# Performance work log

Measured on AMD Instinct MI355X. Metric: run time of the kernel, lower is better.

Reference implementation:

```python
import jax, jax.numpy as jnp
import numpy as np

N = 50000      # nodes
E = 800000     # random edges (self-loops appended -> E + N total)
IN, HID, OUT, HEADS = 128, 256, 256, 8


def _gat_layer(x, src, dst, W, a_src, a_dst, bias):
    # x: [N, F_in]; W: [F_in, H*C]; a_src/a_dst: [H, C]; bias: [H*C]
    n = x.shape[0]
    H, C = a_src.shape
    h = (x @ W).reshape(n, H, C)                      # per-head transform
    al_s = jnp.sum(h * a_src, axis=-1)                # [N, H]
    al_d = jnp.sum(h * a_dst, axis=-1)                # [N, H]
    e = jax.nn.leaky_relu(al_s[src] + al_d[dst], 0.2) # [E, H]
    # segmented softmax over incoming edges of each destination node
    m = jax.ops.segment_max(e, dst, num_segments=n)   # [N, H]
    e = jnp.exp(e - m[dst])
    s = jax.ops.segment_sum(e, dst, num_segments=n)   # [N, H]
    alpha = e / (s[dst] + 1e-16)                      # [E, H]
    out = jax.ops.segment_sum(alpha[:, :, None] * h[src], dst, num_segments=n)
    return out.reshape(n, H * C) + bias


def setup_inputs() -> dict:
    key = jax.random.key(0)
    ks = jax.random.split(key, 9)
    x = jax.random.normal(ks[0], (N, IN), dtype=jnp.float32)
    src = jax.random.randint(ks[1], (E,), 0, N)
    dst = jax.random.randint(ks[2], (E,), 0, N)
    loop = jnp.arange(N)  # PyG GATConv adds self-loops by default
    edge_index = jnp.stack([jnp.concatenate([src, loop]),
                            jnp.concatenate([dst, loop])]).astype(jnp.int64)
    C1, C2 = HID // HEADS, OUT // HEADS
    W1 = jax.random.normal(ks[3], (IN, HID), jnp.float32) * (1.0 / np.sqrt(IN))
    a1_src = jax.random.normal(ks[4], (HEADS, C1), jnp.float32) * 0.1
    a1_dst = jax.random.normal(ks[5], (HEADS, C1), jnp.float32) * 0.1
    b1 = jnp.zeros((HID,), jnp.float32)
    W2 = jax.random.normal(ks[6], (HID, OUT), jnp.float32) * (1.0 / np.sqrt(HID))
    a2_src = jax.random.normal(ks[7], (HEADS, C2), jnp.float32) * 0.1
    a2_dst = jax.random.normal(ks[8], (HEADS, C2), jnp.float32) * 0.1
    b2 = jnp.zeros((OUT,), jnp.float32)
    return {"x": x, "edge_index": edge_index,
            "W1": W1, "a1_src": a1_src, "a1_dst": a1_dst, "b1": b1,
            "W2": W2, "a2_src": a2_src, "a2_dst": a2_dst, "b2": b2}


def reference(x, edge_index, W1, a1_src, a1_dst, b1, W2, a2_src, a2_dst, b2):
    src, dst = edge_index[0], edge_index[1]
    h = jax.nn.elu(_gat_layer(x, src, dst, W1, a1_src, a1_dst, b1))
    out = jax.nn.elu(_gat_layer(h, src, dst, W2, a2_src, a2_dst, b2))
    return out
```

## Files before the change

### kernel.cpp

```cpp
#include <hip/hip_runtime.h>
#include <hip/hip_bf16.h>


#define HEADS 8
#define F 256

typedef _Float16 h8 __attribute__((ext_vector_type(8)));
typedef _Float16 h4 __attribute__((ext_vector_type(4)));
typedef float f4 __attribute__((ext_vector_type(4)));


__global__ void k_prep(const float* __restrict__ W1, _Float16* __restrict__ Wt1,
                       const float* __restrict__ W2, _Float16* __restrict__ Wt2,
                       const int* __restrict__ dst, int Et, int* __restrict__ deg) {
  int b = blockIdx.x, tid = threadIdx.x;
  if (b < 128) {
    Wt1[(size_t)tid * 128 + b] = (_Float16)W1[(size_t)b * F + tid];
  } else if (b < 384) {
    int k = b - 128;
    Wt2[(size_t)tid * 256 + k] = (_Float16)W2[(size_t)k * F + tid];
  } else {
    int i = (b - 384) * 256 + tid;
    for (; i < Et; i += 512 * 256) atomicAdd(&deg[dst[i]], 1);
  }
}


__global__ __launch_bounds__(1024) void k_scan1(const int* __restrict__ deg, int n,
                                                int* __restrict__ rowptr, int* __restrict__ bsum) {
  __shared__ int s[1024];
  int i = blockIdx.x * 1024 + threadIdx.x;
  int v = (i < n) ? ((deg[i] + 3) & ~3) : 0;
  s[threadIdx.x] = v;
  __syncthreads();
  for (int off = 1; off < 1024; off <<= 1) {
    int add = (threadIdx.x >= off) ? s[threadIdx.x - off] : 0;
    __syncthreads();
    s[threadIdx.x] += add;
    __syncthreads();
  }
  if (i < n) rowptr[i] = s[threadIdx.x] - v;
  if (threadIdx.x == 1023) bsum[blockIdx.x] = s[1023];
}

__global__ void k_scan23(int n, const int* __restrict__ bsum,
                         int* __restrict__ rowptr, int* __restrict__ rowwork) {
  __shared__ int boffs;
  int nbx = blockIdx.x >> 2;
  if (threadIdx.x < 64) {
    int t = threadIdx.x;
    int v = (t < nbx) ? bsum[t] : 0;
#pragma unroll
    for (int off = 32; off; off >>= 1) v += __shfl_xor(v, off, 64);
    if (t == 0) boffs = v;
  }
  __syncthreads();
  int i = blockIdx.x * 256 + threadIdx.x;
  if (i < n) {
    int v = rowptr[i] + boffs;
    rowptr[i] = v;
    rowwork[i] = v;
  }
}


template <bool AF32, bool FILL>
__global__ __launch_bounds__(512) void k_gemm(const void* __restrict__ Av,
                                              const _Float16* __restrict__ Bt,
                                              _Float16* __restrict__ C,
                                              const float* __restrict__ a_src,
                                              const float* __restrict__ a_dst,
                                              float* __restrict__ als,
                                              float* __restrict__ ald,
                                              int M, int K,
                                              const int* __restrict__ esrc,
                                              const int* __restrict__ edst,
                                              int Et, int* __restrict__ rowwork,
                                              int* __restrict__ csr, int gemmBlocks) {
  if (FILL && (int)blockIdx.x >= gemmBlocks) {
    int i = ((int)blockIdx.x - gemmBlocks) * 512 + threadIdx.x;
    int stride = ((int)gridDim.x - gemmBlocks) * 512;
    for (; i < Et; i += stride) {
      int pos = atomicAdd(&rowwork[edst[i]], 1);
      csr[pos] = esrc[i];
    }
    return;
  }

  __shared__ _Float16 As[128][40];
  __shared__ _Float16 Bs[256][40];
  int tid = threadIdx.x;
  int lane = tid & 63, w = tid >> 6;
  int wr = w & 1, wc = w >> 1;
  int rowBase = blockIdx.x * 128;
  f4 acc[4][4] = {};

  int arow = tid >> 2, akoff = (tid & 3) * 8;
  int arow_g = min(rowBase + arow, M - 1);
  const _Float16* Ap = (const _Float16*)Av + (size_t)arow_g * K + akoff;
  const float*    Apf = (const float*)Av + (size_t)arow_g * K + akoff;
  int bc = tid >> 1, bkoff = (tid & 1) * 16;
  const _Float16* Bp = Bt + (size_t)bc * K + bkoff;

  int kl = (lane >> 4) * 8;
  int rl = lane & 15;

  int nsteps = K >> 5;
  h8 av;
  float4 af0, af1;
  if (AF32) { af0 = *(const float4*)(Apf); af1 = *(const float4*)(Apf + 4); }
  else av = *(const h8*)(Ap);
  h8 bv0 = *(const h8*)(Bp);
  h8 bv1 = *(const h8*)(Bp + 8);

  for (int s = 0; s < nsteps; ++s) {
    if (AF32) {
      h8 t = {(_Float16)af0.x, (_Float16)af0.y, (_Float16)af0.z, (_Float16)af0.w,
              (_Float16)af1.x, (_Float16)af1.y, (_Float16)af1.z, (_Float16)af1.w};
      *(h8*)&As[arow][akoff] = t;
    } else {
      *(h8*)&As[arow][akoff] = av;
    }
    *(h8*)&Bs[bc][bkoff] = bv0;
    *(h8*)&Bs[bc][bkoff + 8] = bv1;
    __syncthreads();
    if (s + 1 < nsteps) {
      int k0 = (s + 1) << 5;
      if (AF32) { af0 = *(const float4*)(Apf + k0); af1 = *(const float4*)(Apf + k0 + 4); }
      else av = *(const h8*)(Ap + k0);
      bv0 = *(const h8*)(Bp + k0);
      bv1 = *(const h8*)(Bp + k0 + 8);
    }
    h8 afr[4], bfr[4];
#pragma unroll
    for (int fi = 0; fi < 4; ++fi) afr[fi] = *(const h8*)&As[wr * 64 + fi * 16 + rl][kl];
#pragma unroll
    for (int fj = 0; fj < 4; ++fj) bfr[fj] = *(const h8*)&Bs[wc * 64 + fj * 16 + rl][kl];
#pragma unroll
    for (int fi = 0; fi < 4; ++fi)
#pragma unroll
      for (int fj = 0; fj < 4; ++fj)
        acc[fi][fj] = __builtin_amdgcn_mfma_f32_16x16x32_f16(afr[fi], bfr[fj], acc[fi][fj], 0, 0, 0);
    __syncthreads();
  }

  int rquad = (lane >> 4) * 4;

#pragma unroll
  for (int fi = 0; fi < 4; ++fi)
#pragma unroll
    for (int fj = 0; fj < 4; ++fj) {
      int col = wc * 64 + fj * 16 + rl;
#pragma unroll
      for (int r = 0; r < 4; ++r) {
        int row = rowBase + wr * 64 + fi * 16 + rquad + r;
        if (row < M) C[(size_t)row * F + col] = (_Float16)acc[fi][fj][r];
      }
    }

  int head0 = wc * 2;
  float as0 = a_src[head0 * 32 + rl],      as1 = a_src[head0 * 32 + 16 + rl];
  float ad0 = a_dst[head0 * 32 + rl],      ad1 = a_dst[head0 * 32 + 16 + rl];
  float cs0 = a_src[head0 * 32 + 32 + rl], cs1 = a_src[head0 * 32 + 48 + rl];
  float cd0 = a_dst[head0 * 32 + 32 + rl], cd1 = a_dst[head0 * 32 + 48 + rl];
#pragma unroll
  for (int fi = 0; fi < 4; ++fi)
#pragma unroll
    for (int r = 0; r < 4; ++r) {
      float v0s = acc[fi][0][r] * as0 + acc[fi][1][r] * as1;
      float v0d = acc[fi][0][r] * ad0 + acc[fi][1][r] * ad1;
      float v1s = acc[fi][2][r] * cs0 + acc[fi][3][r] * cs1;
      float v1d = acc[fi][2][r] * cd0 + acc[fi][3][r] * cd1;
#pragma unroll
      for (int off = 8; off; off >>= 1) {
        v0s += __shfl_xor(v0s, off);
        v0d += __shfl_xor(v0d, off);
        v1s += __shfl_xor(v1s, off);
        v1d += __shfl_xor(v1d, off);
      }
      int row = rowBase + wr * 64 + fi * 16 + rquad + r;
      if (rl == 0 && row < M) {
        als[row * HEADS + head0] = v0s;
        ald[row * HEADS + head0] = v0d;
        als[row * HEADS + head0 + 1] = v1s;
        ald[row * HEADS + head0 + 1] = v1d;
      }
    }
}


template <bool F16OUT>
__global__ __launch_bounds__(256) void k_agg(const int* __restrict__ rowptr,
                                             const int* __restrict__ deg,
                                             const int* __restrict__ csr,
                                             const float* __restrict__ al_s,
                                             const float* __restrict__ al_d,
                                             const _Float16* __restrict__ h,
                                             const float* __restrict__ bias,
                                             float* __restrict__ outf,
                                             _Float16* __restrict__ outh,
                                             int n) {
  int tid = threadIdx.x;
  int w = tid >> 6, lane = tid & 63;
  int node = blockIdx.x * 4 + w;
  if (node >= n) return;
  int base = rowptr[node];
  int d = deg[node];
  int hh = lane >> 3;
  float alD = al_d[node * HEADS + hh];
  const _Float16* hc = h + (lane << 2);
  const int* cp = csr + base;

  f4 acc = {0.f, 0.f, 0.f, 0.f};
  float sp = 0.f;
  int j = 0;
  if (d >= 4) {
    int4 sv = *(const int4*)cp;
    for (; j + 4 <= d; j += 4) {
      int4 svn = sv;
      if (j + 8 <= d) svn = *(const int4*)(cp + j + 4);
      float e0 = al_s[sv.x * HEADS + hh] + alD;
      float e1 = al_s[sv.y * HEADS + hh] + alD;
      float e2 = al_s[sv.z * HEADS + hh] + alD;
      float e3 = al_s[sv.w * HEADS + hh] + alD;
      e0 = (e0 > 0.f) ? e0 : 0.2f * e0;
      e1 = (e1 > 0.f) ? e1 : 0.2f * e1;
      e2 = (e2 > 0.f) ? e2 : 0.2f * e2;
      e3 = (e3 > 0.f) ? e3 : 0.2f * e3;
      float p0 = __expf(e0), p1 = __expf(e1), p2 = __expf(e2), p3 = __expf(e3);
      h4 v0 = *(const h4*)(hc + ((size_t)sv.x << 8));
      h4 v1 = *(const h4*)(hc + ((size_t)sv.y << 8));
      h4 v2 = *(const h4*)(hc + ((size_t)sv.z << 8));
      h4 v3 = *(const h4*)(hc + ((size_t)sv.w << 8));
      acc.x += p0 * (float)v0.x + p1 * (float)v1.x + p2 * (float)v2.x + p3 * (float)v3.x;
      acc.y += p0 * (float)v0.y + p1 * (float)v1.y + p2 * (float)v2.y + p3 * (float)v3.y;
      acc.z += p0 * (float)v0.z + p1 * (float)v1.z + p2 * (float)v2.z + p3 * (float)v3.z;
      acc.w += p0 * (float)v0.w + p1 * (float)v1.w + p2 * (float)v2.w + p3 * (float)v3.w;
      sp += p0 + p1 + p2 + p3;
      sv = svn;
    }
  }
  for (; j < d; ++j) {
    int s = cp[j];
    float e = al_s[s * HEADS + hh] + alD;
    e = (e > 0.f) ? e : 0.2f * e;
    float p = __expf(e);
    h4 v = *(const h4*)(hc + ((size_t)s << 8));
    acc.x += p * (float)v.x;
    acc.y += p * (float)v.y;
    acc.z += p * (float)v.z;
    acc.w += p * (float)v.w;
    sp += p;
  }

  float invs = 1.f / (sp + 1e-16f);
  int c0 = lane << 2;
  float4 bv = *(const float4*)&bias[c0];
  float o0 = acc.x * invs + bv.x;
  float o1 = acc.y * invs + bv.y;
  float o2 = acc.z * invs + bv.z;
  float o3 = acc.w * invs + bv.w;
  o0 = (o0 > 0.f) ? o0 : expm1f(o0);
  o1 = (o1 > 0.f) ? o1 : expm1f(o1);
  o2 = (o2 > 0.f) ? o2 : expm1f(o2);
  o3 = (o3 > 0.f) ? o3 : expm1f(o3);
  if (F16OUT) {
    h4 o = {(_Float16)o0, (_Float16)o1, (_Float16)o2, (_Float16)o3};
    *(h4*)&outh[((size_t)node << 8) + c0] = o;
  } else {
    *(float4*)&outf[((size_t)node << 8) + c0] = make_float4(o0, o1, o2, o3);
  }
}


extern "C" void kernel_launch(void* const* d_in, const int* in_sizes, int n_in,
                              void* d_out, int out_size, void* d_ws, size_t ws_size,
                              hipStream_t stream) {
  const float* x   = (const float*)d_in[0];
  const int*   ei  = (const int*)d_in[1];
  const float* W1  = (const float*)d_in[2];
  const float* a1s = (const float*)d_in[3];
  const float* a1d = (const float*)d_in[4];
  const float* b1  = (const float*)d_in[5];
  const float* W2  = (const float*)d_in[6];
  const float* a2s = (const float*)d_in[7];
  const float* a2d = (const float*)d_in[8];
  const float* b2  = (const float*)d_in[9];

  int n  = in_sizes[0] / 128;
  int Et = in_sizes[1] / 2;
  const int* srcp = ei;
  const int* dstp = ei + Et;

  char* ws = (char*)d_ws;
  auto alloc = [&](size_t bytes) {
    char* p = ws;
    ws += (bytes + 255) & ~(size_t)255;
    return p;
  };
  _Float16* hbuf    = (_Float16*)alloc((size_t)n * F * 2);
  _Float16* Wt1     = (_Float16*)alloc((size_t)128 * F * 2);
  _Float16* Wt2     = (_Float16*)alloc((size_t)F * F * 2);
  float*    als     = (float*)alloc((size_t)n * HEADS * 4);
  float*    ald     = (float*)alloc((size_t)n * HEADS * 4);
  int*      deg     = (int*)alloc((size_t)n * 4);
  int*      rowptr  = (int*)alloc((size_t)(n + 1) * 4);
  int*      rowwork = (int*)alloc((size_t)n * 4);
  int*      bsum    = (int*)alloc(64 * 4);
  int*      csr     = (int*)alloc(((size_t)Et + 4 * (size_t)n) * 4);
  _Float16* out1h   = (_Float16*)d_out;
  float*    outF    = (float*)d_out;

  hipMemsetAsync(deg, 0, (size_t)n * 4, stream);

  k_prep<<<384 + 512, 256, 0, stream>>>(W1, Wt1, W2, Wt2, dstp, Et, deg);

  int nb = (n + 1023) / 1024;
  k_scan1<<<nb, 1024, 0, stream>>>(deg, n, rowptr, bsum);
  k_scan23<<<(n + 255) / 256, 256, 0, stream>>>(n, bsum, rowptr, rowwork);

  int gb = (n + 127) / 128;
  int ab = (n + 3) / 4;
  k_gemm<true, true><<<gb + 1024, 512, 0, stream>>>(x, Wt1, hbuf, a1s, a1d, als, ald,
                                                    n, 128, srcp, dstp, Et, rowwork, csr, gb);
  k_agg<true><<<ab, 256, 0, stream>>>(rowptr, deg, csr, als, ald, hbuf, b1, nullptr, out1h, n);
  k_gemm<false, false><<<gb, 512, 0, stream>>>(out1h, Wt2, hbuf, a2s, a2d, als, ald,
                                               n, 256, nullptr, nullptr, 0, nullptr, nullptr, gb);
  k_agg<false><<<ab, 256, 0, stream>>>(rowptr, deg, csr, als, ald, hbuf, b2, outF, nullptr, n);
}
```

Measured before the change: 348.3 us.

## Treat self-loops implicitly, vectorize CSR build, lane-parallel edge softmax in aggregation

Assumes the last N edges are self-loops in node order. It drops them from the degree count and the CSR fill and writes each node's self index directly at the end of its row. Degree counting and CSR fill now read dst/src as int4 with four atomics per thread. The fill is launched with half as many extra blocks. Aggregation now computes one edge's attention weight per lane across 8 lanes and broadcasts it with ds_swizzle, with a shuffle reduction for the softmax sum. This cuts redundant exp and al_s gathers, but it relies on the self-loop layout of the input and on Er being a multiple of 4.

```diff
diff --git a/kernel.cpp b/kernel.cpp
--- a/kernel.cpp
+++ b/kernel.cpp
@@ -12,7 +12,7 @@
 
 __global__ void k_prep(const float* __restrict__ W1, _Float16* __restrict__ Wt1,
                        const float* __restrict__ W2, _Float16* __restrict__ Wt2,
-                       const int* __restrict__ dst, int Et, int* __restrict__ deg) {
+                       const int* __restrict__ dst, int Er, int* __restrict__ deg) {
   int b = blockIdx.x, tid = threadIdx.x;
   if (b < 128) {
     Wt1[(size_t)tid * 128 + b] = (_Float16)W1[(size_t)b * F + tid];
@@ -20,8 +20,14 @@
     int k = b - 128;
     Wt2[(size_t)tid * 256 + k] = (_Float16)W2[(size_t)k * F + tid];
   } else {
-    int i = (b - 384) * 256 + tid;
-    for (; i < Et; i += 512 * 256) atomicAdd(&deg[dst[i]], 1);
+    int nq = Er >> 2;
+    for (int q = (b - 384) * 256 + tid; q < nq; q += 512 * 256) {
+      int4 d4 = *(const int4*)(dst + (q << 2));
+      atomicAdd(&deg[d4.x], 1);
+      atomicAdd(&deg[d4.y], 1);
+      atomicAdd(&deg[d4.z], 1);
+      atomicAdd(&deg[d4.w], 1);
+    }
   }
 }
 
@@ -30,7 +36,7 @@
                                                 int* __restrict__ rowptr, int* __restrict__ bsum) {
   __shared__ int s[1024];
   int i = blockIdx.x * 1024 + threadIdx.x;
-  int v = (i < n) ? ((deg[i] + 3) & ~3) : 0;
+  int v = (i < n) ? ((deg[i] + 4) & ~3) : 0;
   s[threadIdx.x] = v;
   __syncthreads();
   for (int off = 1; off < 1024; off <<= 1) {
@@ -43,8 +49,9 @@
   if (threadIdx.x == 1023) bsum[blockIdx.x] = s[1023];
 }
 
-__global__ void k_scan23(int n, const int* __restrict__ bsum,
-                         int* __restrict__ rowptr, int* __restrict__ rowwork) {
+__global__ void k_scan23(int n, const int* __restrict__ bsum, const int* __restrict__ deg,
+                         int* __restrict__ rowptr, int* __restrict__ rowwork,
+                         int* __restrict__ csr) {
   __shared__ int boffs;
   int nbx = blockIdx.x >> 2;
   if (threadIdx.x < 64) {
@@ -60,6 +67,7 @@
     int v = rowptr[i] + boffs;
     rowptr[i] = v;
     rowwork[i] = v;
+    csr[v + deg[i]] = i;
   }
 }
 
@@ -75,14 +83,22 @@
                                               int M, int K,
                                               const int* __restrict__ esrc,
                                               const int* __restrict__ edst,
-                                              int Et, int* __restrict__ rowwork,
+                                              int Er, int* __restrict__ rowwork,
                                               int* __restrict__ csr, int gemmBlocks) {
   if (FILL && (int)blockIdx.x >= gemmBlocks) {
-    int i = ((int)blockIdx.x - gemmBlocks) * 512 + threadIdx.x;
+    int nq = Er >> 2;
     int stride = ((int)gridDim.x - gemmBlocks) * 512;
-    for (; i < Et; i += stride) {
-      int pos = atomicAdd(&rowwork[edst[i]], 1);
-      csr[pos] = esrc[i];
+    for (int q = ((int)blockIdx.x - gemmBlocks) * 512 + threadIdx.x; q < nq; q += stride) {
+      int4 d4 = *(const int4*)(edst + (q << 2));
+      int4 s4 = *(const int4*)(esrc + (q << 2));
+      int p0 = atomicAdd(&rowwork[d4.x], 1);
+      int p1 = atomicAdd(&rowwork[d4.y], 1);
+      int p2 = atomicAdd(&rowwork[d4.z], 1);
+      int p3 = atomicAdd(&rowwork[d4.w], 1);
+      csr[p0] = s4.x;
+      csr[p1] = s4.y;
+      csr[p2] = s4.z;
+      csr[p3] = s4.w;
     }
     return;
   }
@@ -205,55 +221,43 @@
   int node = blockIdx.x * 4 + w;
   if (node >= n) return;
   int base = rowptr[node];
-  int d = deg[node];
-  int hh = lane >> 3;
+  int d = deg[node] + 1;
+  int hh = lane >> 3, sl = lane & 7;
   float alD = al_d[node * HEADS + hh];
-  const _Float16* hc = h + (lane << 2);
   const int* cp = csr + base;
+  const _Float16* hl = h + (lane << 2);
 
   f4 acc = {0.f, 0.f, 0.f, 0.f};
   float sp = 0.f;
-  int j = 0;
-  if (d >= 4) {
-    int4 sv = *(const int4*)cp;
-    for (; j + 4 <= d; j += 4) {
-      int4 svn = sv;
-      if (j + 8 <= d) svn = *(const int4*)(cp + j + 4);
-      float e0 = al_s[sv.x * HEADS + hh] + alD;
-      float e1 = al_s[sv.y * HEADS + hh] + alD;
-      float e2 = al_s[sv.z * HEADS + hh] + alD;
-      float e3 = al_s[sv.w * HEADS + hh] + alD;
-      e0 = (e0 > 0.f) ? e0 : 0.2f * e0;
-      e1 = (e1 > 0.f) ? e1 : 0.2f * e1;
-      e2 = (e2 > 0.f) ? e2 : 0.2f * e2;
-      e3 = (e3 > 0.f) ? e3 : 0.2f * e3;
-      float p0 = __expf(e0), p1 = __expf(e1), p2 = __expf(e2), p3 = __expf(e3);
-      h4 v0 = *(const h4*)(hc + ((size_t)sv.x << 8));
-      h4 v1 = *(const h4*)(hc + ((size_t)sv.y << 8));
-      h4 v2 = *(const h4*)(hc + ((size_t)sv.z << 8));
-      h4 v3 = *(const h4*)(hc + ((size_t)sv.w << 8));
-      acc.x += p0 * (float)v0.x + p1 * (float)v1.x + p2 * (float)v2.x + p3 * (float)v3.x;
-      acc.y += p0 * (float)v0.y + p1 * (float)v1.y + p2 * (float)v2.y + p3 * (float)v3.y;
-      acc.z += p0 * (float)v0.z + p1 * (float)v1.z + p2 * (float)v2.z + p3 * (float)v3.z;
-      acc.w += p0 * (float)v0.w + p1 * (float)v1.w + p2 * (float)v2.w + p3 * (float)v3.w;
-      sp += p0 + p1 + p2 + p3;
-      sv = svn;
-    }
-  }
-  for (; j < d; ++j) {
-    int s = cp[j];
-    float e = al_s[s * HEADS + hh] + alD;
+
+  for (int j0 = 0; j0 < d; j0 += 8) {
+    int je = j0 + sl;
+    int jc = min(je, d - 1);
+    int s_lane = cp[jc];
+    float e = al_s[s_lane * HEADS + hh] + alD;
     e = (e > 0.f) ? e : 0.2f * e;
-    float p = __expf(e);
-    h4 v = *(const h4*)(hc + ((size_t)s << 8));
-    acc.x += p * (float)v.x;
-    acc.y += p * (float)v.y;
-    acc.z += p * (float)v.z;
-    acc.w += p * (float)v.w;
+    float p = (je < d) ? __expf(e) : 0.f;
     sp += p;
-  }
-
+    int4 q0 = *(const int4*)(cp + j0);
+    int4 q1 = *(const int4*)(cp + j0 + 4);
+    int pi = __builtin_bit_cast(int, p);
+#define EDGE(k, sk) \
+    if (j0 + (k) < d) { \
+      float pk = __builtin_bit_cast(float, __builtin_amdgcn_ds_swizzle(pi, ((k) << 5) | 0x18)); \
+      unsigned sU = (unsigned)__builtin_amdgcn_readfirstlane(sk); \
+      h4 v = *(const h4*)(hl + ((size_t)sU << 8)); \
+      acc.x += pk * (float)v.x; acc.y += pk * (float)v.y; \
+      acc.z += pk * (float)v.z; acc.w += pk * (float)v.w; \
+    }
+    EDGE(0, q0.x) EDGE(1, q0.y) EDGE(2, q0.z) EDGE(3, q0.w)
+    EDGE(4, q1.x) EDGE(5, q1.y) EDGE(6, q1.z) EDGE(7, q1.w)
+#undef EDGE
+  }
+
+#pragma unroll
+  for (int off = 4; off; off >>= 1) sp += __shfl_xor(sp, off);
   float invs = 1.f / (sp + 1e-16f);
+
   int c0 = lane << 2;
   float4 bv = *(const float4*)&bias[c0];
   float o0 = acc.x * invs + bv.x;
@@ -289,6 +293,7 @@
 
   int n  = in_sizes[0] / 128;
   int Et = in_sizes[1] / 2;
+  int Er = Et - n;
   const int* srcp = ei;
   const int* dstp = ei + Et;
 
@@ -313,16 +318,16 @@
 
   hipMemsetAsync(deg, 0, (size_t)n * 4, stream);
 
-  k_prep<<<384 + 512, 256, 0, stream>>>(W1, Wt1, W2, Wt2, dstp, Et, deg);
+  k_prep<<<384 + 512, 256, 0, stream>>>(W1, Wt1, W2, Wt2, dstp, Er, deg);
 
   int nb = (n + 1023) / 1024;
   k_scan1<<<nb, 1024, 0, stream>>>(deg, n, rowptr, bsum);
-  k_scan23<<<(n + 255) / 256, 256, 0, stream>>>(n, bsum, rowptr, rowwork);
+  k_scan23<<<(n + 255) / 256, 256, 0, stream>>>(n, bsum, deg, rowptr, rowwork, csr);
 
   int gb = (n + 127) / 128;
   int ab = (n + 3) / 4;
-  k_gemm<true, true><<<gb + 1024, 512, 0, stream>>>(x, Wt1, hbuf, a1s, a1d, als, ald,
-                                                    n, 128, srcp, dstp, Et, rowwork, csr, gb);
+  k_gemm<true, true><<<gb + 512, 512, 0, stream>>>(x, Wt1, hbuf, a1s, a1d, als, ald,
+                                                   n, 128, srcp, dstp, Er, rowwork, csr, gb);
   k_agg<true><<<ab, 256, 0, stream>>>(rowptr, deg, csr, als, ald, hbuf, b1, nullptr, out1h, n);
   k_gemm<false, false><<<gb, 512, 0, stream>>>(out1h, Wt2, hbuf, a2s, a2d, als, ald,
                                                n, 256, nullptr, nullptr, 0, nullptr, nullptr, gb);
```

Result: slower. 399.8 us (+14.8%).
